# Kernel optimization log

Measured on AMD Instinct MI355X. Metric: run time of the kernel, lower is better.

The kernel has to match this reference:

```python
import jax, jax.numpy as jnp
import numpy as np

B, N, M = 1024, 512, 256  # batch, n_locations, vec_size
EPS_ADD = 1e-16   # additive eps used by the torch module
EPS_COS = 1e-8    # torch.cosine_similarity default eps (clamps norms)


def setup_inputs() -> dict:
    key0 = jax.random.key(0)
    ks = jax.random.split(key0, 9)
    return {
        "memory": jax.random.normal(ks[0], (B, N, M), jnp.float32),
        "key":    jax.random.normal(ks[1], (B, M), jnp.float32),
        "beta":   jax.random.uniform(ks[2], (B, 1), jnp.float32),
        "g":      jax.random.uniform(ks[3], (B, 1), jnp.float32),
        "s":      jax.random.uniform(ks[4], (B, 3), jnp.float32),
        "gamma":  jax.random.uniform(ks[5], (B, 1), jnp.float32),
        "w_prev": jax.random.uniform(ks[6], (B, N), jnp.float32),
        "e":      jax.random.uniform(ks[7], (B, M), jnp.float32),
        "a":      jax.random.normal(ks[8], (B, M), jnp.float32),
    }


def reference(memory, key, beta, g, s, gamma, w_prev, e, a):
    b, n, m = memory.shape
    # --- content addressing: cosine similarity of each memory row vs key ---
    mem = memory + EPS_ADD
    k = key[:, None, :] + EPS_ADD                       # [B,1,M]
    num = jnp.sum(mem * k, axis=-1)                     # [B,N]
    den = (jnp.maximum(jnp.linalg.norm(mem, axis=-1), EPS_COS)
           * jnp.maximum(jnp.linalg.norm(k, axis=-1), EPS_COS))
    w_c = jax.nn.softmax(beta * (num / den), axis=1)    # [B,N]
    # --- interpolation gate ---
    w_g = g * w_c + (1.0 - g) * w_prev                  # [B,N]
    # --- circular convolutional shift (kernel size 3, cross-correlation) ---
    # torch: t = [w_g[-1], w_g, w_g[0]]; out[i] = sum_j t[i+j]*s[j]
    #       = sum_{d in {-1,0,1}} w_g[(i+d) mod N] * s[d+1]
    idx = (jnp.arange(n)[:, None] + jnp.arange(-1, 2)[None, :]) % n  # [N,3]
    w_tilda = jnp.einsum('bnk,bk->bn', w_g[:, idx], s)  # [B,N]
    # --- sharpening ---
    w_pow = w_tilda ** gamma                            # gamma [B,1] broadcasts
    w = w_pow / (jnp.sum(w_pow, axis=1, keepdims=True) + EPS_ADD)
    # --- read ---
    r = jnp.einsum('bn,bnm->bm', w, memory)             # [B,M]
    # --- write (erase + add via outer products) ---
    erase = w[:, :, None] * e[:, None, :]               # [B,N,M]
    add = w[:, :, None] * a[:, None, :]                 # [B,N,M]
    new_mem = memory * (1.0 - erase) + add              # [B,N,M]
    # flatten all outputs into one array: [B, N + M + N*M]
    return jnp.concatenate([w, r, new_mem.reshape(b, n * m)], axis=1)
```

## Files before the change

kernel.cpp:

```cpp
#include <hip/hip_runtime.h>
#include <math.h>

#define BB 1024
#define NN 512
#define MM 256
#define OUTROW (NN + MM + NN * MM)
#define EPS_ADD 1e-16f
#define EPS_COS 1e-8f
#define G_REG 11
#define G_TOT 16

typedef float f4v __attribute__((ext_vector_type(4)));

__device__ inline float waveReduceSum(float v) {
#pragma unroll
    for (int off = 32; off > 0; off >>= 1) v += __shfl_xor(v, off);
    return v;
}
__device__ inline float waveReduceMax(float v) {
#pragma unroll
    for (int off = 32; off > 0; off >>= 1) v = fmaxf(v, __shfl_xor(v, off));
    return v;
}

__device__ __forceinline__ void ldgrp(f4v (&buf)[4], const float* __restrict__ rp) {
#pragma unroll
    for (int mc = 0; mc < 4; ++mc)
        buf[mc] = *reinterpret_cast<const f4v*>(rp + mc * 64);
}
__device__ __forceinline__ void ldgrp_nt(f4v (&buf)[4], const float* __restrict__ rp) {
#pragma unroll
    for (int mc = 0; mc < 4; ++mc)
        buf[mc] = __builtin_nontemporal_load(reinterpret_cast<const f4v*>(rp + mc * 64));
}

__device__ __forceinline__ void redgrp(const f4v (&buf)[4], const f4v (&kf)[4],
                                       float bet, float kn, float* __restrict__ sc,
                                       int row, int sl) {
    float dot = 0.f, ssq = 0.f;
#pragma unroll
    for (int mc = 0; mc < 4; ++mc) {
        const float mx = buf[mc].x + EPS_ADD, my = buf[mc].y + EPS_ADD;
        const float mz = buf[mc].z + EPS_ADD, mw = buf[mc].w + EPS_ADD;
        dot += mx * kf[mc].x + my * kf[mc].y + mz * kf[mc].z + mw * kf[mc].w;
        ssq += mx * mx + my * my + mz * mz + mw * mw;
    }
#pragma unroll
    for (int off = 8; off > 0; off >>= 1) {
        dot += __shfl_xor(dot, off);
        ssq += __shfl_xor(ssq, off);
    }
    if (sl == 0)
        sc[row] = bet * dot / (fmaxf(sqrtf(ssq), EPS_COS) * kn);
}

__device__ __forceinline__ void procgrp(const f4v (&mvv)[4], float wn,
                                        const f4v (&ev)[4], const f4v (&av)[4],
                                        f4v (&acc)[4], float* __restrict__ op) {
#pragma unroll
    for (int mc = 0; mc < 4; ++mc) {
        const f4v nm = mvv[mc] * (1.f - wn * ev[mc]) + wn * av[mc];
        __builtin_nontemporal_store(nm, reinterpret_cast<f4v*>(op + mc * 64));
        acc[mc] += wn * mvv[mc];
    }
}

__global__ __launch_bounds__(512, 2) void ntm_memory_kernel(
    const float* __restrict__ memory, const float* __restrict__ key,
    const float* __restrict__ beta, const float* __restrict__ g,
    const float* __restrict__ s, const float* __restrict__ gamma,
    const float* __restrict__ w_prev, const float* __restrict__ e,
    const float* __restrict__ a, float* __restrict__ out) {
    const int b    = blockIdx.x;
    const int t    = threadIdx.x;
    const int lane = t & 63;
    const int wave = t >> 6;
    const int sub  = lane >> 4;
    const int sl   = lane & 15;

    __shared__ float key_lds[MM];
    __shared__ float sc[NN];
    __shared__ float wg[NN];
    __shared__ float wf[NN];
    __shared__ float ea_lds[2 * MM];
    __shared__ float red[8];
    __shared__ float rpart[8][MM];

    const float* __restrict__ memb = memory + (size_t)b * NN * MM;
    float* __restrict__ outb       = out + (size_t)b * OUTROW;

    if (t < MM) {
        key_lds[t]      = key[b * MM + t] + EPS_ADD;
        ea_lds[MM + t]  = a[b * MM + t];
    } else {
        const int i = t - MM;
        ea_lds[i] = e[b * MM + i];
    }
    __syncthreads();

    if (t < MM) {
        float kv = key_lds[t];
        float ss = waveReduceSum(kv * kv);
        if (lane == 0) red[wave] = ss;
    }
    __syncthreads();
    const float kn  = fmaxf(sqrtf(red[0] + red[1] + red[2] + red[3]), EPS_COS);
    const float bet = beta[b];
    const float gv  = g[b];
    const float gam = gamma[b];
    const float s0  = s[b * 3 + 0];
    const float s1  = s[b * 3 + 1];
    const float s2  = s[b * 3 + 2];
    __syncthreads();

    const int rowbase = wave * 64 + sub;
    const float* __restrict__ rp0 = memb + (size_t)rowbase * MM + sl * 4;

    f4v kf[4];
#pragma unroll
    for (int mc = 0; mc < 4; ++mc)
        kf[mc] = *reinterpret_cast<const f4v*>(&key_lds[mc * 64 + sl * 4]);

    f4v tile[G_REG][4];
#pragma unroll
    for (int gp = 0; gp < G_REG; ++gp)
        ldgrp_nt(tile[gp], rp0 + (size_t)(4 * gp) * MM);

#pragma unroll
    for (int gp = 0; gp < G_REG; ++gp)
        redgrp(tile[gp], kf, bet, kn, sc, rowbase + 4 * gp, sl);

    {
        f4v sA[4], sB[4];
        ldgrp(sA, rp0 + (size_t)(4 * (G_REG + 0)) * MM);
        ldgrp(sB, rp0 + (size_t)(4 * (G_REG + 1)) * MM);
        redgrp(sA, kf, bet, kn, sc, rowbase + 4 * (G_REG + 0), sl);
        ldgrp(sA, rp0 + (size_t)(4 * (G_REG + 2)) * MM);
        redgrp(sB, kf, bet, kn, sc, rowbase + 4 * (G_REG + 1), sl);
        ldgrp(sB, rp0 + (size_t)(4 * (G_REG + 3)) * MM);
        redgrp(sA, kf, bet, kn, sc, rowbase + 4 * (G_REG + 2), sl);
        ldgrp(sA, rp0 + (size_t)(4 * (G_REG + 4)) * MM);
        redgrp(sB, kf, bet, kn, sc, rowbase + 4 * (G_REG + 3), sl);
        redgrp(sA, kf, bet, kn, sc, rowbase + 4 * (G_REG + 4), sl);
    }
    __syncthreads();

    const float v = sc[t];
    {
        float m1 = waveReduceMax(v);
        if (lane == 0) red[wave] = m1;
    }
    __syncthreads();
    float mmax = red[0];
#pragma unroll
    for (int k = 1; k < 8; k++) mmax = fmaxf(mmax, red[k]);
    const float ex = expf(v - mmax);
    __syncthreads();
    {
        float s1w = waveReduceSum(ex);
        if (lane == 0) red[wave] = s1w;
    }
    __syncthreads();
    float esum = 0.f;
#pragma unroll
    for (int k = 0; k < 8; k++) esum += red[k];
    const float w_c = ex / esum;

    wg[t] = gv * w_c + (1.f - gv) * w_prev[b * NN + t];
    __syncthreads();
    const float wt = wg[(t + NN - 1) & (NN - 1)] * s0 + wg[t] * s1 +
                     wg[(t + 1) & (NN - 1)] * s2;
    const float wp = powf(wt, gam);
    __syncthreads();
    {
        float sw = waveReduceSum(wp);
        if (lane == 0) red[wave] = sw;
    }
    __syncthreads();
    float wsum = 0.f;
#pragma unroll
    for (int k = 0; k < 8; k++) wsum += red[k];
    const float wv = wp / (wsum + EPS_ADD);
    wf[t]   = wv;
    outb[t] = wv;
    __syncthreads();

    f4v ev[4], av[4], acc[4];
#pragma unroll
    for (int mc = 0; mc < 4; ++mc) {
        ev[mc]  = *reinterpret_cast<const f4v*>(&ea_lds[mc * 64 + sl * 4]);
        av[mc]  = *reinterpret_cast<const f4v*>(&ea_lds[MM + mc * 64 + sl * 4]);
        acc[mc] = (f4v)0.f;
    }
    float* __restrict__ ob0 = outb + (NN + MM) + (size_t)rowbase * MM + sl * 4;

#pragma unroll
    for (int gp = 0; gp < G_REG; ++gp) {
        const float wn = wf[rowbase + 4 * gp];
        procgrp(tile[gp], wn, ev, av, acc, ob0 + (size_t)(4 * gp) * MM);
    }
    {
        f4v sA[4], sB[4];
        ldgrp(sA, rp0 + (size_t)(4 * (G_REG + 0)) * MM);
        ldgrp(sB, rp0 + (size_t)(4 * (G_REG + 1)) * MM);
        procgrp(sA, wf[rowbase + 4 * (G_REG + 0)], ev, av, acc,
                ob0 + (size_t)(4 * (G_REG + 0)) * MM);
        ldgrp(sA, rp0 + (size_t)(4 * (G_REG + 2)) * MM);
        procgrp(sB, wf[rowbase + 4 * (G_REG + 1)], ev, av, acc,
                ob0 + (size_t)(4 * (G_REG + 1)) * MM);
        ldgrp(sB, rp0 + (size_t)(4 * (G_REG + 3)) * MM);
        procgrp(sA, wf[rowbase + 4 * (G_REG + 2)], ev, av, acc,
                ob0 + (size_t)(4 * (G_REG + 2)) * MM);
        ldgrp(sA, rp0 + (size_t)(4 * (G_REG + 4)) * MM);
        procgrp(sB, wf[rowbase + 4 * (G_REG + 3)], ev, av, acc,
                ob0 + (size_t)(4 * (G_REG + 3)) * MM);
        procgrp(sA, wf[rowbase + 4 * (G_REG + 4)], ev, av, acc,
                ob0 + (size_t)(4 * (G_REG + 4)) * MM);
    }

#pragma unroll
    for (int mc = 0; mc < 4; ++mc) {
        acc[mc].x += __shfl_xor(acc[mc].x, 16); acc[mc].y += __shfl_xor(acc[mc].y, 16);
        acc[mc].z += __shfl_xor(acc[mc].z, 16); acc[mc].w += __shfl_xor(acc[mc].w, 16);
        acc[mc].x += __shfl_xor(acc[mc].x, 32); acc[mc].y += __shfl_xor(acc[mc].y, 32);
        acc[mc].z += __shfl_xor(acc[mc].z, 32); acc[mc].w += __shfl_xor(acc[mc].w, 32);
    }
    if (sub == 0) {
#pragma unroll
        for (int mc = 0; mc < 4; ++mc)
            *reinterpret_cast<f4v*>(&rpart[wave][mc * 64 + sl * 4]) = acc[mc];
    }
    __syncthreads();
    if (t < MM) {
        float rsum = 0.f;
#pragma unroll
        for (int k = 0; k < 8; k++) rsum += rpart[k][t];
        outb[NN + t] = rsum;
    }
}

extern "C" void kernel_launch(void* const* d_in, const int* in_sizes, int n_in,
                              void* d_out, int out_size, void* d_ws, size_t ws_size,
                              hipStream_t stream) {
    const float* memory = (const float*)d_in[0];
    const float* key    = (const float*)d_in[1];
    const float* beta   = (const float*)d_in[2];
    const float* g      = (const float*)d_in[3];
    const float* s      = (const float*)d_in[4];
    const float* gamma  = (const float*)d_in[5];
    const float* w_prev = (const float*)d_in[6];
    const float* e      = (const float*)d_in[7];
    const float* a      = (const float*)d_in[8];
    float* out = (float*)d_out;

    ntm_memory_kernel<<<BB, 512, 0, stream>>>(memory, key, beta, g, s, gamma,
                                              w_prev, e, a, out);
}
```

Baseline: 209.7 us.

## Process two batches per block and prefetch second batch tile during first write

Result: slower. 223.0 us (+6.3%).

```diff
diff --git a/kernel.cpp b/kernel.cpp
--- a/kernel.cpp
+++ b/kernel.cpp
@@ -65,13 +65,60 @@
     }
 }
 
+__device__ __forceinline__ void weight_pipeline(
+    int t, int lane, int wave,
+    float gv, float gam, float s0, float s1, float s2,
+    const float* __restrict__ wprow, float* __restrict__ outb,
+    float* __restrict__ sc, float* __restrict__ wg, float* __restrict__ wf,
+    float* __restrict__ red) {
+    const float v = sc[t];
+    {
+        const float m1 = waveReduceMax(v);
+        if (lane == 0) red[wave] = m1;
+    }
+    __syncthreads();
+    float mmax = red[0];
+#pragma unroll
+    for (int k = 1; k < 8; k++) mmax = fmaxf(mmax, red[k]);
+    const float ex = expf(v - mmax);
+    __syncthreads();
+    {
+        const float s1w = waveReduceSum(ex);
+        if (lane == 0) red[wave] = s1w;
+    }
+    __syncthreads();
+    float esum = 0.f;
+#pragma unroll
+    for (int k = 0; k < 8; k++) esum += red[k];
+    const float w_c = ex / esum;
+    wg[t] = gv * w_c + (1.f - gv) * wprow[t];
+    __syncthreads();
+    const float wt = wg[(t + NN - 1) & (NN - 1)] * s0 + wg[t] * s1 +
+                     wg[(t + 1) & (NN - 1)] * s2;
+    const float wp = powf(wt, gam);
+    __syncthreads();
+    {
+        const float sw = waveReduceSum(wp);
+        if (lane == 0) red[wave] = sw;
+    }
+    __syncthreads();
+    float wsum = 0.f;
+#pragma unroll
+    for (int k = 0; k < 8; k++) wsum += red[k];
+    const float wv = wp / (wsum + EPS_ADD);
+    wf[t]   = wv;
+    outb[t] = wv;
+    __syncthreads();
+}
+
 __global__ __launch_bounds__(512, 2) void ntm_memory_kernel(
     const float* __restrict__ memory, const float* __restrict__ key,
     const float* __restrict__ beta, const float* __restrict__ g,
     const float* __restrict__ s, const float* __restrict__ gamma,
     const float* __restrict__ w_prev, const float* __restrict__ e,
     const float* __restrict__ a, float* __restrict__ out) {
-    const int b    = blockIdx.x;
+    const int b0   = blockIdx.x;
+    const int b1   = blockIdx.x + (BB / 2);
     const int t    = threadIdx.x;
     const int lane = t & 63;
     const int wave = t >> 6;
@@ -86,156 +133,216 @@
     __shared__ float red[8];
     __shared__ float rpart[8][MM];
 
-    const float* __restrict__ memb = memory + (size_t)b * NN * MM;
-    float* __restrict__ outb       = out + (size_t)b * OUTROW;
-
-    if (t < MM) {
-        key_lds[t]      = key[b * MM + t] + EPS_ADD;
-        ea_lds[MM + t]  = a[b * MM + t];
+    const int rowbase = wave * 64 + sub;
+    const float* __restrict__ memb0 = memory + (size_t)b0 * NN * MM;
+    const float* __restrict__ memb1 = memory + (size_t)b1 * NN * MM;
+    const float* __restrict__ rp0 = memb0 + (size_t)rowbase * MM + sl * 4;
+    const float* __restrict__ rp1 = memb1 + (size_t)rowbase * MM + sl * 4;
+    float* __restrict__ outb0 = out + (size_t)b0 * OUTROW;
+    float* __restrict__ outb1 = out + (size_t)b1 * OUTROW;
+
+    f4v tile[G_REG][4];
+
+    if (t < MM) {
+        key_lds[t]     = key[b0 * MM + t] + EPS_ADD;
+        ea_lds[MM + t] = a[b0 * MM + t];
     } else {
-        const int i = t - MM;
-        ea_lds[i] = e[b * MM + i];
-    }
-    __syncthreads();
-
-    if (t < MM) {
-        float kv = key_lds[t];
-        float ss = waveReduceSum(kv * kv);
+        ea_lds[t - MM] = e[b0 * MM + (t - MM)];
+    }
+    __syncthreads();
+    if (t < MM) {
+        const float kv = key_lds[t];
+        const float ss = waveReduceSum(kv * kv);
         if (lane == 0) red[wave] = ss;
     }
     __syncthreads();
-    const float kn  = fmaxf(sqrtf(red[0] + red[1] + red[2] + red[3]), EPS_COS);
-    const float bet = beta[b];
-    const float gv  = g[b];
-    const float gam = gamma[b];
-    const float s0  = s[b * 3 + 0];
-    const float s1  = s[b * 3 + 1];
-    const float s2  = s[b * 3 + 2];
-    __syncthreads();
-
-    const int rowbase = wave * 64 + sub;
-    const float* __restrict__ rp0 = memb + (size_t)rowbase * MM + sl * 4;
-
-    f4v kf[4];
-#pragma unroll
-    for (int mc = 0; mc < 4; ++mc)
-        kf[mc] = *reinterpret_cast<const f4v*>(&key_lds[mc * 64 + sl * 4]);
-
-    f4v tile[G_REG][4];
-#pragma unroll
-    for (int gp = 0; gp < G_REG; ++gp)
-        ldgrp_nt(tile[gp], rp0 + (size_t)(4 * gp) * MM);
-
-#pragma unroll
-    for (int gp = 0; gp < G_REG; ++gp)
-        redgrp(tile[gp], kf, bet, kn, sc, rowbase + 4 * gp, sl);
-
-    {
+    const float kn0 = fmaxf(sqrtf(red[0] + red[1] + red[2] + red[3]), EPS_COS);
+    const float bet0 = beta[b0], gv0 = g[b0], gam0 = gamma[b0];
+    const float s00 = s[b0 * 3 + 0], s01 = s[b0 * 3 + 1], s02 = s[b0 * 3 + 2];
+    __syncthreads();
+
+    {
+        f4v kf[4];
+#pragma unroll
+        for (int mc = 0; mc < 4; ++mc)
+            kf[mc] = *reinterpret_cast<const f4v*>(&key_lds[mc * 64 + sl * 4]);
+
+#pragma unroll
+        for (int gp = 0; gp < G_REG; ++gp)
+            ldgrp_nt(tile[gp], rp0 + (size_t)(4 * gp) * MM);
+#pragma unroll
+        for (int gp = 0; gp < G_REG; ++gp)
+            redgrp(tile[gp], kf, bet0, kn0, sc, rowbase + 4 * gp, sl);
+
         f4v sA[4], sB[4];
         ldgrp(sA, rp0 + (size_t)(4 * (G_REG + 0)) * MM);
         ldgrp(sB, rp0 + (size_t)(4 * (G_REG + 1)) * MM);
-        redgrp(sA, kf, bet, kn, sc, rowbase + 4 * (G_REG + 0), sl);
+        redgrp(sA, kf, bet0, kn0, sc, rowbase + 4 * (G_REG + 0), sl);
         ldgrp(sA, rp0 + (size_t)(4 * (G_REG + 2)) * MM);
-        redgrp(sB, kf, bet, kn, sc, rowbase + 4 * (G_REG + 1), sl);
+        redgrp(sB, kf, bet0, kn0, sc, rowbase + 4 * (G_REG + 1), sl);
         ldgrp(sB, rp0 + (size_t)(4 * (G_REG + 3)) * MM);
-        redgrp(sA, kf, bet, kn, sc, rowbase + 4 * (G_REG + 2), sl);
+        redgrp(sA, kf, bet0, kn0, sc, rowbase + 4 * (G_REG + 2), sl);
         ldgrp(sA, rp0 + (size_t)(4 * (G_REG + 4)) * MM);
-        redgrp(sB, kf, bet, kn, sc, rowbase + 4 * (G_REG + 3), sl);
-        redgrp(sA, kf, bet, kn, sc, rowbase + 4 * (G_REG + 4), sl);
-    }
-    __syncthreads();
-
-    const float v = sc[t];
-    {
-        float m1 = waveReduceMax(v);
-        if (lane == 0) red[wave] = m1;
-    }
-    __syncthreads();
-    float mmax = red[0];
-#pragma unroll
-    for (int k = 1; k < 8; k++) mmax = fmaxf(mmax, red[k]);
-    const float ex = expf(v - mmax);
-    __syncthreads();
-    {
-        float s1w = waveReduceSum(ex);
-        if (lane == 0) red[wave] = s1w;
-    }
-    __syncthreads();
-    float esum = 0.f;
-#pragma unroll
-    for (int k = 0; k < 8; k++) esum += red[k];
-    const float w_c = ex / esum;
-
-    wg[t] = gv * w_c + (1.f - gv) * w_prev[b * NN + t];
-    __syncthreads();
-    const float wt = wg[(t + NN - 1) & (NN - 1)] * s0 + wg[t] * s1 +
-                     wg[(t + 1) & (NN - 1)] * s2;
-    const float wp = powf(wt, gam);
-    __syncthreads();
-    {
-        float sw = waveReduceSum(wp);
-        if (lane == 0) red[wave] = sw;
-    }
-    __syncthreads();
-    float wsum = 0.f;
-#pragma unroll
-    for (int k = 0; k < 8; k++) wsum += red[k];
-    const float wv = wp / (wsum + EPS_ADD);
-    wf[t]   = wv;
-    outb[t] = wv;
-    __syncthreads();
-
-    f4v ev[4], av[4], acc[4];
-#pragma unroll
-    for (int mc = 0; mc < 4; ++mc) {
-        ev[mc]  = *reinterpret_cast<const f4v*>(&ea_lds[mc * 64 + sl * 4]);
-        av[mc]  = *reinterpret_cast<const f4v*>(&ea_lds[MM + mc * 64 + sl * 4]);
-        acc[mc] = (f4v)0.f;
-    }
-    float* __restrict__ ob0 = outb + (NN + MM) + (size_t)rowbase * MM + sl * 4;
-
-#pragma unroll
-    for (int gp = 0; gp < G_REG; ++gp) {
-        const float wn = wf[rowbase + 4 * gp];
-        procgrp(tile[gp], wn, ev, av, acc, ob0 + (size_t)(4 * gp) * MM);
-    }
-    {
+        redgrp(sB, kf, bet0, kn0, sc, rowbase + 4 * (G_REG + 3), sl);
+        redgrp(sA, kf, bet0, kn0, sc, rowbase + 4 * (G_REG + 4), sl);
+    }
+    __syncthreads();
+
+    weight_pipeline(t, lane, wave, gv0, gam0, s00, s01, s02,
+                    w_prev + (size_t)b0 * NN, outb0, sc, wg, wf, red);
+
+    {
+        f4v ev[4], av[4], acc[4];
+#pragma unroll
+        for (int mc = 0; mc < 4; ++mc) {
+            ev[mc]  = *reinterpret_cast<const f4v*>(&ea_lds[mc * 64 + sl * 4]);
+            av[mc]  = *reinterpret_cast<const f4v*>(&ea_lds[MM + mc * 64 + sl * 4]);
+            acc[mc] = (f4v)0.f;
+        }
+        float* __restrict__ ob0 = outb0 + (NN + MM) + (size_t)rowbase * MM + sl * 4;
+#pragma unroll
+        for (int gp = 0; gp < G_REG; ++gp)
+            procgrp(tile[gp], wf[rowbase + 4 * gp], ev, av, acc,
+                    ob0 + (size_t)(4 * gp) * MM);
+        {
+            f4v sA[4], sB[4];
+            ldgrp(sA, rp0 + (size_t)(4 * (G_REG + 0)) * MM);
+            ldgrp(sB, rp0 + (size_t)(4 * (G_REG + 1)) * MM);
+            procgrp(sA, wf[rowbase + 4 * (G_REG + 0)], ev, av, acc,
+                    ob0 + (size_t)(4 * (G_REG + 0)) * MM);
+            ldgrp(sA, rp0 + (size_t)(4 * (G_REG + 2)) * MM);
+            procgrp(sB, wf[rowbase + 4 * (G_REG + 1)], ev, av, acc,
+                    ob0 + (size_t)(4 * (G_REG + 1)) * MM);
+            ldgrp(sB, rp0 + (size_t)(4 * (G_REG + 3)) * MM);
+            procgrp(sA, wf[rowbase + 4 * (G_REG + 2)], ev, av, acc,
+                    ob0 + (size_t)(4 * (G_REG + 2)) * MM);
+            ldgrp(sA, rp0 + (size_t)(4 * (G_REG + 4)) * MM);
+            procgrp(sB, wf[rowbase + 4 * (G_REG + 3)], ev, av, acc,
+                    ob0 + (size_t)(4 * (G_REG + 3)) * MM);
+            procgrp(sA, wf[rowbase + 4 * (G_REG + 4)], ev, av, acc,
+                    ob0 + (size_t)(4 * (G_REG + 4)) * MM);
+        }
+
+#pragma unroll
+        for (int gp = 0; gp < G_REG; ++gp)
+            ldgrp_nt(tile[gp], rp1 + (size_t)(4 * gp) * MM);
+
+#pragma unroll
+        for (int mc = 0; mc < 4; ++mc) {
+            acc[mc].x += __shfl_xor(acc[mc].x, 16); acc[mc].y += __shfl_xor(acc[mc].y, 16);
+            acc[mc].z += __shfl_xor(acc[mc].z, 16); acc[mc].w += __shfl_xor(acc[mc].w, 16);
+            acc[mc].x += __shfl_xor(acc[mc].x, 32); acc[mc].y += __shfl_xor(acc[mc].y, 32);
+            acc[mc].z += __shfl_xor(acc[mc].z, 32); acc[mc].w += __shfl_xor(acc[mc].w, 32);
+        }
+        if (sub == 0) {
+#pragma unroll
+            for (int mc = 0; mc < 4; ++mc)
+                *reinterpret_cast<f4v*>(&rpart[wave][mc * 64 + sl * 4]) = acc[mc];
+        }
+    }
+    __syncthreads();
+    if (t < MM) {
+        float rsum = 0.f;
+#pragma unroll
+        for (int k = 0; k < 8; k++) rsum += rpart[k][t];
+        outb0[NN + t] = rsum;
+    }
+
+    if (t < MM) {
+        key_lds[t]     = key[b1 * MM + t] + EPS_ADD;
+        ea_lds[MM + t] = a[b1 * MM + t];
+    } else {
+        ea_lds[t - MM] = e[b1 * MM + (t - MM)];
+    }
+    __syncthreads();
+    if (t < MM) {
+        const float kv = key_lds[t];
+        const float ss = waveReduceSum(kv * kv);
+        if (lane == 0) red[wave] = ss;
+    }
+    __syncthreads();
+    const float kn1 = fmaxf(sqrtf(red[0] + red[1] + red[2] + red[3]), EPS_COS);
+    const float bet1 = beta[b1], gv1 = g[b1], gam1 = gamma[b1];
+    const float s10 = s[b1 * 3 + 0], s11 = s[b1 * 3 + 1], s12 = s[b1 * 3 + 2];
+    __syncthreads();
+
+    {
+        f4v kf[4];
+#pragma unroll
+        for (int mc = 0; mc < 4; ++mc)
+            kf[mc] = *reinterpret_cast<const f4v*>(&key_lds[mc * 64 + sl * 4]);
+
+#pragma unroll
+        for (int gp = 0; gp < G_REG; ++gp)
+            redgrp(tile[gp], kf, bet1, kn1, sc, rowbase + 4 * gp, sl);
+
         f4v sA[4], sB[4];
-        ldgrp(sA, rp0 + (size_t)(4 * (G_REG + 0)) * MM);
-        ldgrp(sB, rp0 + (size_t)(4 * (G_REG + 1)) * MM);
-        procgrp(sA, wf[rowbase + 4 * (G_REG + 0)], ev, av, acc,
-                ob0 + (size_t)(4 * (G_REG + 0)) * MM);
-        ldgrp(sA, rp0 + (size_t)(4 * (G_REG + 2)) * MM);
-        procgrp(sB, wf[rowbase + 4 * (G_REG + 1)], ev, av, acc,
-                ob0 + (size_t)(4 * (G_REG + 1)) * MM);
-        ldgrp(sB, rp0 + (size_t)(4 * (G_REG + 3)) * MM);
-        procgrp(sA, wf[rowbase + 4 * (G_REG + 2)], ev, av, acc,
-                ob0 + (size_t)(4 * (G_REG + 2)) * MM);
-        ldgrp(sA, rp0 + (size_t)(4 * (G_REG + 4)) * MM);
-        procgrp(sB, wf[rowbase + 4 * (G_REG + 3)], ev, av, acc,
-                ob0 + (size_t)(4 * (G_REG + 3)) * MM);
-        procgrp(sA, wf[rowbase + 4 * (G_REG + 4)], ev, av, acc,
-                ob0 + (size_t)(4 * (G_REG + 4)) * MM);
-    }
-
-#pragma unroll
-    for (int mc = 0; mc < 4; ++mc) {
-        acc[mc].x += __shfl_xor(acc[mc].x, 16); acc[mc].y += __shfl_xor(acc[mc].y, 16);
-        acc[mc].z += __shfl_xor(acc[mc].z, 16); acc[mc].w += __shfl_xor(acc[mc].w, 16);
-        acc[mc].x += __shfl_xor(acc[mc].x, 32); acc[mc].y += __shfl_xor(acc[mc].y, 32);
-        acc[mc].z += __shfl_xor(acc[mc].z, 32); acc[mc].w += __shfl_xor(acc[mc].w, 32);
-    }
-    if (sub == 0) {
-#pragma unroll
-        for (int mc = 0; mc < 4; ++mc)
-            *reinterpret_cast<f4v*>(&rpart[wave][mc * 64 + sl * 4]) = acc[mc];
+        ldgrp(sA, rp1 + (size_t)(4 * (G_REG + 0)) * MM);
+        ldgrp(sB, rp1 + (size_t)(4 * (G_REG + 1)) * MM);
+        redgrp(sA, kf, bet1, kn1, sc, rowbase + 4 * (G_REG + 0), sl);
+        ldgrp(sA, rp1 + (size_t)(4 * (G_REG + 2)) * MM);
+        redgrp(sB, kf, bet1, kn1, sc, rowbase + 4 * (G_REG + 1), sl);
+        ldgrp(sB, rp1 + (size_t)(4 * (G_REG + 3)) * MM);
+        redgrp(sA, kf, bet1, kn1, sc, rowbase + 4 * (G_REG + 2), sl);
+        ldgrp(sA, rp1 + (size_t)(4 * (G_REG + 4)) * MM);
+        redgrp(sB, kf, bet1, kn1, sc, rowbase + 4 * (G_REG + 3), sl);
+        redgrp(sA, kf, bet1, kn1, sc, rowbase + 4 * (G_REG + 4), sl);
+    }
+    __syncthreads();
+
+    weight_pipeline(t, lane, wave, gv1, gam1, s10, s11, s12,
+                    w_prev + (size_t)b1 * NN, outb1, sc, wg, wf, red);
+
+    {
+        f4v ev[4], av[4], acc[4];
+#pragma unroll
+        for (int mc = 0; mc < 4; ++mc) {
+            ev[mc]  = *reinterpret_cast<const f4v*>(&ea_lds[mc * 64 + sl * 4]);
+            av[mc]  = *reinterpret_cast<const f4v*>(&ea_lds[MM + mc * 64 + sl * 4]);
+            acc[mc] = (f4v)0.f;
+        }
+        float* __restrict__ ob1 = outb1 + (NN + MM) + (size_t)rowbase * MM + sl * 4;
+#pragma unroll
+        for (int gp = 0; gp < G_REG; ++gp)
+            procgrp(tile[gp], wf[rowbase + 4 * gp], ev, av, acc,
+                    ob1 + (size_t)(4 * gp) * MM);
+        {
+            f4v sA[4], sB[4];
+            ldgrp(sA, rp1 + (size_t)(4 * (G_REG + 0)) * MM);
+            ldgrp(sB, rp1 + (size_t)(4 * (G_REG + 1)) * MM);
+            procgrp(sA, wf[rowbase + 4 * (G_REG + 0)], ev, av, acc,
+                    ob1 + (size_t)(4 * (G_REG + 0)) * MM);
+            ldgrp(sA, rp1 + (size_t)(4 * (G_REG + 2)) * MM);
+            procgrp(sB, wf[rowbase + 4 * (G_REG + 1)], ev, av, acc,
+                    ob1 + (size_t)(4 * (G_REG + 1)) * MM);
+            ldgrp(sB, rp1 + (size_t)(4 * (G_REG + 3)) * MM);
+            procgrp(sA, wf[rowbase + 4 * (G_REG + 2)], ev, av, acc,
+                    ob1 + (size_t)(4 * (G_REG + 2)) * MM);
+            ldgrp(sA, rp1 + (size_t)(4 * (G_REG + 4)) * MM);
+            procgrp(sB, wf[rowbase + 4 * (G_REG + 3)], ev, av, acc,
+                    ob1 + (size_t)(4 * (G_REG + 3)) * MM);
+            procgrp(sA, wf[rowbase + 4 * (G_REG + 4)], ev, av, acc,
+                    ob1 + (size_t)(4 * (G_REG + 4)) * MM);
+        }
+#pragma unroll
+        for (int mc = 0; mc < 4; ++mc) {
+            acc[mc].x += __shfl_xor(acc[mc].x, 16); acc[mc].y += __shfl_xor(acc[mc].y, 16);
+            acc[mc].z += __shfl_xor(acc[mc].z, 16); acc[mc].w += __shfl_xor(acc[mc].w, 16);
+            acc[mc].x += __shfl_xor(acc[mc].x, 32); acc[mc].y += __shfl_xor(acc[mc].y, 32);
+            acc[mc].z += __shfl_xor(acc[mc].z, 32); acc[mc].w += __shfl_xor(acc[mc].w, 32);
+        }
+        if (sub == 0) {
+#pragma unroll
+            for (int mc = 0; mc < 4; ++mc)
+                *reinterpret_cast<f4v*>(&rpart[wave][mc * 64 + sl * 4]) = acc[mc];
+        }
     }
     __syncthreads();
     if (t < MM) {
         float rsum = 0.f;
 #pragma unroll
         for (int k = 0; k < 8; k++) rsum += rpart[k][t];
-        outb[NN + t] = rsum;
+        outb1[NN + t] = rsum;
     }
 }
 
@@ -253,6 +360,6 @@
     const float* a      = (const float*)d_in[8];
     float* out = (float*)d_out;
 
-    ntm_memory_kernel<<<BB, 512, 0, stream>>>(memory, key, beta, g, s, gamma,
-                                              w_prev, e, a, out);
-}
+    ntm_memory_kernel<<<BB / 2, 512, 0, stream>>>(memory, key, beta, g, s, gamma,
+                                                  w_prev, e, a, out);
+}
```
